# Performance work log

Measured on AMD Instinct MI355X. Metric: run time of the kernel, lower is better.

The kernel has to match this reference:

```python
import jax, jax.numpy as jnp
import numpy as np

N_HEADS = 8
D_EMBED = 512
D_HEAD = D_EMBED // N_HEADS


def setup_inputs() -> dict:
    key = jax.random.key(0)
    ks = jax.random.split(key, 5)
    s = 1.0 / np.sqrt(D_EMBED)
    return {
        "x": jax.random.normal(ks[0], (2, 4096, D_EMBED), dtype=jnp.float32),
        "in_proj_w": jax.random.normal(ks[1], (3 * D_EMBED, D_EMBED), dtype=jnp.float32) * s,
        "in_proj_b": jax.random.normal(ks[2], (3 * D_EMBED,), dtype=jnp.float32) * s,
        "out_proj_w": jax.random.normal(ks[3], (D_EMBED, D_EMBED), dtype=jnp.float32) * s,
        "out_proj_b": jax.random.normal(ks[4], (D_EMBED,), dtype=jnp.float32) * s,
    }


def reference(x, in_proj_w, in_proj_b, out_proj_w, out_proj_b):
    B, S, D = x.shape
    # in_proj: x @ W^T + b, then chunk into q, k, v
    qkv = jnp.einsum("bsd,ed->bse", x, in_proj_w) + in_proj_b  # [B,S,3D]
    q, k, v = jnp.split(qkv, 3, axis=-1)
    # [B,S,D] -> [B,H,S,dh]
    def heads(t):
        return t.reshape(B, S, N_HEADS, D_HEAD).transpose(0, 2, 1, 3)
    q, k, v = heads(q), heads(k), heads(v)
    scale = 1.0 / np.sqrt(D_HEAD).astype(np.float32)
    scores = jnp.einsum("bhqd,bhkd->bhqk", q, k) * scale  # [B,H,S,S]
    attn = jax.nn.softmax(scores, axis=-1)
    out = jnp.einsum("bhqk,bhkd->bhqd", attn, v)  # [B,H,S,dh]
    out = out.transpose(0, 2, 1, 3).reshape(B, S, D)
    return jnp.einsum("bsd,ed->bse", out, out_proj_w) + out_proj_b
```

## Files before the change

kernel.cpp:

```cpp
#include <hip/hip_runtime.h>
#include <cstdint>
#include <cstddef>

typedef __bf16 bf16x8 __attribute__((ext_vector_type(8)));
typedef float f32x4 __attribute__((ext_vector_type(4)));
typedef float f32x16 __attribute__((ext_vector_type(16)));
typedef unsigned int u32x4 __attribute__((ext_vector_type(4)));
typedef int i32x2 __attribute__((ext_vector_type(2)));
typedef unsigned short u16;
typedef unsigned short u16x8 __attribute__((ext_vector_type(8)));
typedef unsigned int u32;

#define S_LEN 4096
#define NH 8
#define DH 64
#define D_EMB 512
#define BATCH 2
#define M_ROWS 8192
#define GK 512
#define QSCALE 0.18033688011112042f

__device__ __forceinline__ u16 f2bf(float f) {
  u32 u = __builtin_bit_cast(u32, f);
  u += 0x7FFFu + ((u >> 16) & 1u);
  return (u16)(u >> 16);
}
__device__ __forceinline__ float bf2f(u16 v) {
  return __builtin_bit_cast(float, (u32)v << 16);
}
__device__ __forceinline__ u32 pk2(float a, float b) {
  union { __bf16 h[2]; u32 w; } u;
  u.h[0] = (__bf16)a;
  u.h[1] = (__bf16)b;
  return u.w;
}
__device__ __forceinline__ float fexp2(float x) {
#if __has_builtin(__builtin_amdgcn_exp2f)
  return __builtin_amdgcn_exp2f(x);
#else
  return __expf(x * 0.6931471805599453f);
#endif
}

__device__ __forceinline__ float xhalf_add(float v) {
#if __has_builtin(__builtin_amdgcn_permlane32_swap)
  const int a = (int)__builtin_bit_cast(u32, v);
  i32x2 r = __builtin_amdgcn_permlane32_swap(a, a, false, false);
  return __builtin_bit_cast(float, (u32)r.x) +
         __builtin_bit_cast(float, (u32)r.y);
#else
  return v + __shfl_xor(v, 32, 64);
#endif
}

#define MFMA32(a, b, c) __builtin_amdgcn_mfma_f32_32x32x16_bf16(a, b, c, 0, 0, 0)

#define GLD_LDS16(gsrc, ldst)                                                        \
  __builtin_amdgcn_global_load_lds(                                                  \
      (const __attribute__((address_space(1))) void*)(gsrc),                         \
      (__attribute__((address_space(3))) void*)(ldst), 16, 0, 0)

__global__ void detect_kernel(const u16* __restrict__ x, int* __restrict__ flag) {
  __shared__ int cnt;
  if (threadIdx.x == 0) cnt = 0;
  __syncthreads();
  int plaus = 0;
  for (int i = threadIdx.x; i < 2048; i += 256) {
    u16 u = x[2 * i];
    int ex = (u >> 7) & 0xFF;
    plaus += (ex >= 100 && ex <= 134) ? 1 : 0;
  }
  atomicAdd(&cnt, plaus);
  __syncthreads();
  if (threadIdx.x == 0) *flag = (cnt > 1024) ? 0 : 1;
}

__global__ void prep_kernel(const void* __restrict__ x, const void* __restrict__ wq,
                            const void* __restrict__ bq, const void* __restrict__ wo,
                            const void* __restrict__ bo,
                            u16* __restrict__ xb, u16* __restrict__ wqb,
                            u16* __restrict__ wob, float* __restrict__ bqf,
                            float* __restrict__ bof, const int* __restrict__ flag) {
  const bool f32 = (*flag != 0);
  const size_t i = (size_t)blockIdx.x * blockDim.x + threadIdx.x;
  if (i < (size_t)M_ROWS * D_EMB)
    xb[i] = f32 ? f2bf(((const float*)x)[i]) : ((const u16*)x)[i];
  if (i < (size_t)3 * D_EMB * D_EMB)
    wqb[i] = f32 ? f2bf(((const float*)wq)[i]) : ((const u16*)wq)[i];
  if (i < (size_t)D_EMB * D_EMB)
    wob[i] = f32 ? f2bf(((const float*)wo)[i]) : ((const u16*)wo)[i];
  if (i < 3 * D_EMB)
    bqf[i] = f32 ? ((const float*)bq)[i] : bf2f(((const u16*)bq)[i]);
  if (i < D_EMB)
    bof[i] = f32 ? ((const float*)bo)[i] : bf2f(((const u16*)bo)[i]);
}

template <int EPI>
__global__ __launch_bounds__(256, 3)
void gemm_bt(const u16* __restrict__ A, const u16* __restrict__ B, int N,
             const float* __restrict__ bias, u16* __restrict__ qout,
             u16* __restrict__ kout, u16* __restrict__ vout, u16* __restrict__ obf,
             float* __restrict__ of32, const int* __restrict__ flag) {
  __shared__ u16 As[128 * 64];
  __shared__ u16 Bs[128 * 64];
  const int tid = threadIdx.x;
  const int wave = tid >> 6, lane = tid & 63;
  const int m0 = blockIdx.x * 128;
  const int n0 = blockIdx.y * 128;
  const int wr = (wave >> 1) * 64, wc = (wave & 1) * 64;

  const int sr = wave * 8 + (lane >> 3);
  const int scb = (lane & 7) * 16;

  f32x4 acc[4][4] = {};

  for (int k0 = 0; k0 < GK; k0 += 64) {
#pragma unroll
    for (int i = 0; i < 4; ++i) {
      const int r = i * 32 + sr;
      const int sc = (scb ^ ((r & 7) << 4)) >> 1;
      GLD_LDS16(A + (size_t)(m0 + r) * GK + k0 + sc, As + i * 2048 + wave * 512);
    }
#pragma unroll
    for (int i = 0; i < 4; ++i) {
      const int r = i * 32 + sr;
      const int sc = (scb ^ ((r & 7) << 4)) >> 1;
      GLD_LDS16(B + (size_t)(n0 + r) * GK + k0 + sc, Bs + i * 2048 + wave * 512);
    }
    __syncthreads();
#pragma unroll
    for (int kk = 0; kk < 2; ++kk) {
      const int cb = kk * 64 + ((lane >> 4) << 4);
      bf16x8 a[4], b[4];
#pragma unroll
      for (int m = 0; m < 4; ++m) {
        const int r = wr + m * 16 + (lane & 15);
        a[m] = *(const bf16x8*)((const char*)As + r * 128 + (cb ^ ((r & 7) << 4)));
      }
#pragma unroll
      for (int n = 0; n < 4; ++n) {
        const int r = wc + n * 16 + (lane & 15);
        b[n] = *(const bf16x8*)((const char*)Bs + r * 128 + (cb ^ ((r & 7) << 4)));
      }
#pragma unroll
      for (int m = 0; m < 4; ++m)
#pragma unroll
        for (int n = 0; n < 4; ++n)
          acc[m][n] = __builtin_amdgcn_mfma_f32_16x16x32_bf16(a[m], b[n], acc[m][n], 0, 0, 0);
    }
    __syncthreads();
  }

  const bool f32out = (EPI == 1) && (*flag != 0);
#pragma unroll
  for (int n = 0; n < 4; ++n) {
    const int col = n0 + wc + n * 16 + (lane & 15);
    const float bv = bias[col];
#pragma unroll
    for (int m = 0; m < 4; ++m) {
#pragma unroll
      for (int r = 0; r < 4; ++r) {
        const int row = m0 + wr + m * 16 + ((lane >> 4) << 2) + r;
        float v = acc[m][n][r] + bv;
        if (EPI == 0) {
          const int bb = row >> 12, s = row & 4095;
          const int which = col >> 9, hc = col & 511;
          const int h = hc >> 6, d = hc & 63;
          const int bh = bb * NH + h;
          if (which == 2) {
            const int t16 = s >> 4, dblk = d >> 5;
            const int lane_ = ((s >> 3) & 1) * 32 + (d & 31);
            const int j = s & 7;
            vout[(((size_t)(bh * 256 + t16) * 2 + dblk) * 64 + lane_) * 8 + j] = f2bf(v);
          } else {
            const int t32 = s >> 5, dk = d >> 4;
            const int lane_ = ((d >> 3) & 1) * 32 + (s & 31);
            const int j = d & 7;
            u16* dst = (which == 0) ? qout : kout;
            const float vv = (which == 0) ? v * QSCALE : v;
            dst[(((size_t)(bh * 128 + t32) * 4 + dk) * 64 + lane_) * 8 + j] = f2bf(vv);
          }
        } else {
          if (f32out)
            of32[(size_t)row * D_EMB + col] = v;
          else
            obf[(size_t)row * D_EMB + col] = f2bf(v);
        }
      }
    }
  }
}

__global__ __launch_bounds__(256, 4)
void flash_attn(const u16* __restrict__ qfrag, const u16* __restrict__ kfrag,
                const u16* __restrict__ vfrag, u16* __restrict__ ao) {
  __shared__ float Ols[32][65];
  __shared__ float Lsh[4][32];

  const int phys = blockIdx.x;
  const int xcd = phys & 7, slot = phys >> 3;
  const int bh = xcd * 2 + (slot >> 7);
  const int qi = slot & 127;
  const int b = bh >> 3, h = bh & 7;
  const int q0 = qi * 32;

  const int lane = threadIdx.x & 63;
  const int hf = threadIdx.x >> 6;
  const int l31 = lane & 31, hi = lane >> 5;

  bf16x8 qf[4];
  {
    const u16* qb_ = qfrag + ((size_t)(bh * 128 + qi) * 4) * 512 + lane * 8;
#pragma unroll
    for (int dk = 0; dk < 4; ++dk) qf[dk] = *(const bf16x8*)(qb_ + dk * 512);
  }

  const u16* kptr = kfrag + (size_t)bh * (128 * 4 * 512) +
                    (size_t)(hf * 32) * 4 * 512 + lane * 8;
  const u16* vptr = vfrag + (size_t)bh * (256 * 2 * 512) +
                    (size_t)(hf * 64) * 2 * 512 + lane * 8;

  f32x16 accO0 = {}, accO1 = {};
  float lsum = 0.f;

#pragma unroll 1
  for (int it = 0; it < 32; ++it) {
    bf16x8 kf[4], vfA[2], vfB[2];
#pragma unroll
    for (int dk = 0; dk < 4; ++dk)
      kf[dk] = *(const bf16x8*)(kptr + dk * 512);
    vfA[0] = *(const bf16x8*)(vptr);
    vfB[0] = *(const bf16x8*)(vptr + 512);
    vfA[1] = *(const bf16x8*)(vptr + 1024);
    vfB[1] = *(const bf16x8*)(vptr + 1536);
    kptr += 2048;
    vptr += 2048;

    f32x16 s = {};
#pragma unroll
    for (int dk = 0; dk < 4; ++dk) s = MFMA32(kf[dk], qf[dk], s);

#pragma unroll
    for (int i = 0; i < 16; ++i) s[i] = fexp2(s[i]);

    float sm8[8];
#pragma unroll
    for (int i = 0; i < 8; ++i) sm8[i] = s[i] + s[i + 8];
    float sm4[4];
#pragma unroll
    for (int i = 0; i < 4; ++i) sm4[i] = sm8[i] + sm8[i + 4];
    const float sown = (sm4[0] + sm4[1]) + (sm4[2] + sm4[3]);
    lsum += xhalf_add(sown);

    u32 W0, W1, W2, W3;
#if __has_builtin(__builtin_amdgcn_permlane32_swap)
#define PACK8(P, B0)                                                            \
    {                                                                           \
      const u32 w0 = pk2(P[B0 + 0], P[B0 + 1]);                                 \
      const u32 w1 = pk2(P[B0 + 2], P[B0 + 3]);                                 \
      const u32 w2 = pk2(P[B0 + 4], P[B0 + 5]);                                 \
      const u32 w3 = pk2(P[B0 + 6], P[B0 + 7]);                                 \
      i32x2 rA = __builtin_amdgcn_permlane32_swap((int)w0, (int)w2, false, false); \
      i32x2 rB = __builtin_amdgcn_permlane32_swap((int)w1, (int)w3, false, false); \
      W0 = (u32)rA.x; W2 = (u32)rA.y;                                           \
      W1 = (u32)rB.x; W3 = (u32)rB.y;                                           \
    }
#else
#define PACK8(P, B0)                                                   \
    {                                                                  \
      const u32 w0 = pk2(P[B0 + 0], P[B0 + 1]);                        \
      const u32 w1 = pk2(P[B0 + 2], P[B0 + 3]);                        \
      const u32 w2 = pk2(P[B0 + 4], P[B0 + 5]);                        \
      const u32 w3 = pk2(P[B0 + 6], P[B0 + 7]);                        \
      const u32 rA = (u32)__shfl_xor((int)(hi ? w0 : w2), 32, 64);     \
      const u32 rB = (u32)__shfl_xor((int)(hi ? w1 : w3), 32, 64);     \
      W0 = hi ? rA : w0;                                               \
      W1 = hi ? rB : w1;                                               \
      W2 = hi ? w2 : rA;                                               \
      W3 = hi ? w3 : rB;                                               \
    }
#endif

    bf16x8 pa;
    PACK8(s, 0);
    pa = __builtin_bit_cast(bf16x8, (u32x4){W0, W1, W2, W3});
    accO0 = MFMA32(pa, vfA[0], accO0);
    accO1 = MFMA32(pa, vfB[0], accO1);
    PACK8(s, 8);
    pa = __builtin_bit_cast(bf16x8, (u32x4){W0, W1, W2, W3});
    accO0 = MFMA32(pa, vfA[1], accO0);
    accO1 = MFMA32(pa, vfB[1], accO1);
#undef PACK8
  }

  if (hi == 0) Lsh[hf][l31] = lsum;
  __syncthreads();
  const float L = (Lsh[0][l31] + Lsh[1][l31]) + (Lsh[2][l31] + Lsh[3][l31]);
  const float w = 1.0f / L;

#define DEPOSIT(OP)                                                    \
  {                                                                    \
    _Pragma("unroll")                                                  \
    for (int r = 0; r < 16; ++r) {                                     \
      const int qrow = (r & 3) + 8 * (r >> 2) + 4 * hi;                \
      Ols[qrow][l31] OP accO0[r];                                      \
      Ols[qrow][32 + l31] OP accO1[r];                                 \
    }                                                                  \
  }

  if (hf == 0) DEPOSIT(=);
  __syncthreads();
  if (hf == 1) DEPOSIT(+=);
  __syncthreads();
  if (hf == 2) DEPOSIT(+=);
  __syncthreads();
  if (hf == 3) {
#pragma unroll
    for (int r = 0; r < 16; ++r) {
      const int qrow = (r & 3) + 8 * (r >> 2) + 4 * hi;
      const float wr_ = __shfl(w, qrow, 64);
      const float o0 = (accO0[r] + Ols[qrow][l31]) * wr_;
      const float o1 = (accO1[r] + Ols[qrow][32 + l31]) * wr_;
      u16* orow = ao + (size_t)(b * S_LEN + q0 + qrow) * D_EMB + h * DH;
      orow[l31] = f2bf(o0);
      orow[32 + l31] = f2bf(o1);
    }
  }
#undef DEPOSIT
}

extern "C" void kernel_launch(void* const* d_in, const int* in_sizes, int n_in,
                              void* d_out, int out_size, void* d_ws, size_t ws_size,
                              hipStream_t stream) {
  char* w = (char*)d_ws;
  int* flag = (int*)w;
  u16* xb = (u16*)(w + 256);
  u16* wqb = (u16*)(w + 8388864);
  u16* wob = (u16*)(w + 9961728);
  float* bqf = (float*)(w + 10486016);
  float* bof = (float*)(w + 10492160);
  u16* qfr = (u16*)(w + 10494208);
  u16* kfr = (u16*)(w + 18882816);
  u16* vfr = (u16*)(w + 27271424);
  u16* ao = (u16*)(w + 35660032);

  detect_kernel<<<1, 256, 0, stream>>>((const u16*)d_in[0], flag);
  prep_kernel<<<16384, 256, 0, stream>>>(d_in[0], d_in[1], d_in[2], d_in[3], d_in[4],
                                         xb, wqb, wob, bqf, bof, flag);
  gemm_bt<0><<<dim3(64, 12), 256, 0, stream>>>(xb, wqb, 3 * D_EMB, bqf, qfr, kfr, vfr,
                                               nullptr, nullptr, flag);
  flash_attn<<<2048, 256, 0, stream>>>(qfr, kfr, vfr, ao);
  gemm_bt<1><<<dim3(64, 4), 256, 0, stream>>>(ao, wob, D_EMB, bof, nullptr, nullptr,
                                              nullptr, (u16*)d_out, (float*)d_out, flag);
}
```

Before: 147.0 us.

## Rebalance flash attention to 128-query blocks with 2-way KV split; skip bf16 copies

The attention kernel now launches 512 blocks of 512 threads. Each block has four query groups of 32 rows, and each group splits the keys across two waves that each walk 64 iterations. Before, every 32-query block split the keys four ways. The change cuts the cross-wave reduction to one shared-memory deposit and one barrier pair, and it lets the four query groups in a block share K/V loads through the cache. Separately, when the inputs are already bf16, the prep kernel no longer copies x and the weights, and the GEMMs read the raw inputs directly. The longer per-wave loop reduces parallelism per query, and the larger shared-memory footprint may limit occupancy.

```diff
diff --git a/kernel.cpp b/kernel.cpp
--- a/kernel.cpp
+++ b/kernel.cpp
@@ -83,26 +83,31 @@
                             float* __restrict__ bof, const int* __restrict__ flag) {
   const bool f32 = (*flag != 0);
   const size_t i = (size_t)blockIdx.x * blockDim.x + threadIdx.x;
-  if (i < (size_t)M_ROWS * D_EMB)
-    xb[i] = f32 ? f2bf(((const float*)x)[i]) : ((const u16*)x)[i];
-  if (i < (size_t)3 * D_EMB * D_EMB)
-    wqb[i] = f32 ? f2bf(((const float*)wq)[i]) : ((const u16*)wq)[i];
-  if (i < (size_t)D_EMB * D_EMB)
-    wob[i] = f32 ? f2bf(((const float*)wo)[i]) : ((const u16*)wo)[i];
-  if (i < 3 * D_EMB)
-    bqf[i] = f32 ? ((const float*)bq)[i] : bf2f(((const u16*)bq)[i]);
-  if (i < D_EMB)
-    bof[i] = f32 ? ((const float*)bo)[i] : bf2f(((const u16*)bo)[i]);
+  if (!f32) {
+    if (i < 3 * D_EMB) bqf[i] = bf2f(((const u16*)bq)[i]);
+    if (i < D_EMB) bof[i] = bf2f(((const u16*)bo)[i]);
+    return;
+  }
+  if (i < (size_t)M_ROWS * D_EMB) xb[i] = f2bf(((const float*)x)[i]);
+  if (i < (size_t)3 * D_EMB * D_EMB) wqb[i] = f2bf(((const float*)wq)[i]);
+  if (i < (size_t)D_EMB * D_EMB) wob[i] = f2bf(((const float*)wo)[i]);
+  if (i < 3 * D_EMB) bqf[i] = ((const float*)bq)[i];
+  if (i < D_EMB) bof[i] = ((const float*)bo)[i];
 }
 
 template <int EPI>
 __global__ __launch_bounds__(256, 3)
-void gemm_bt(const u16* __restrict__ A, const u16* __restrict__ B, int N,
+void gemm_bt(const u16* __restrict__ Acvt, const void* __restrict__ Araw,
+             const u16* __restrict__ Bcvt, const void* __restrict__ Braw, int N,
              const float* __restrict__ bias, u16* __restrict__ qout,
              u16* __restrict__ kout, u16* __restrict__ vout, u16* __restrict__ obf,
              float* __restrict__ of32, const int* __restrict__ flag) {
   __shared__ u16 As[128 * 64];
   __shared__ u16 Bs[128 * 64];
+  const bool f32in = (*flag != 0);
+  const u16* A = f32in ? Acvt : (const u16*)Araw;
+  const u16* B = f32in ? Bcvt : (const u16*)Braw;
+
   const int tid = threadIdx.x;
   const int wave = tid >> 6, lane = tid & 63;
   const int m0 = blockIdx.x * 128;
@@ -151,7 +156,7 @@
     __syncthreads();
   }
 
-  const bool f32out = (EPI == 1) && (*flag != 0);
+  const bool f32out = (EPI == 1) && f32in;
 #pragma unroll
   for (int n = 0; n < 4; ++n) {
     const int col = n0 + wc + n * 16 + (lane & 15);
@@ -191,40 +196,39 @@
   }
 }
 
-__global__ __launch_bounds__(256, 4)
+__global__ __launch_bounds__(512, 4)
 void flash_attn(const u16* __restrict__ qfrag, const u16* __restrict__ kfrag,
                 const u16* __restrict__ vfrag, u16* __restrict__ ao) {
-  __shared__ float Ols[32][65];
-  __shared__ float Lsh[4][32];
+  __shared__ float Ols[4][32][65];
+  __shared__ float Lsh[4][2][32];
 
   const int phys = blockIdx.x;
   const int xcd = phys & 7, slot = phys >> 3;
-  const int bh = xcd * 2 + (slot >> 7);
-  const int qi = slot & 127;
+  const int bh = xcd * 2 + (slot >> 5);
+  const int qt = slot & 31;
   const int b = bh >> 3, h = bh & 7;
-  const int q0 = qi * 32;
 
   const int lane = threadIdx.x & 63;
-  const int hf = threadIdx.x >> 6;
+  const int w8 = threadIdx.x >> 6;
+  const int g = w8 & 3, hf = w8 >> 2;
   const int l31 = lane & 31, hi = lane >> 5;
+  const int q0 = qt * 128 + g * 32;
 
   bf16x8 qf[4];
   {
-    const u16* qb_ = qfrag + ((size_t)(bh * 128 + qi) * 4) * 512 + lane * 8;
+    const u16* qb_ = qfrag + ((size_t)(bh * 128 + (q0 >> 5)) * 4) * 512 + lane * 8;
 #pragma unroll
     for (int dk = 0; dk < 4; ++dk) qf[dk] = *(const bf16x8*)(qb_ + dk * 512);
   }
 
-  const u16* kptr = kfrag + (size_t)bh * (128 * 4 * 512) +
-                    (size_t)(hf * 32) * 4 * 512 + lane * 8;
-  const u16* vptr = vfrag + (size_t)bh * (256 * 2 * 512) +
-                    (size_t)(hf * 64) * 2 * 512 + lane * 8;
+  const u16* kptr = kfrag + ((size_t)(bh * 128 + hf * 64) * 4) * 512 + lane * 8;
+  const u16* vptr = vfrag + ((size_t)(bh * 256 + hf * 128) * 2) * 512 + lane * 8;
 
   f32x16 accO0 = {}, accO1 = {};
   float lsum = 0.f;
 
 #pragma unroll 1
-  for (int it = 0; it < 32; ++it) {
+  for (int it = 0; it < 64; ++it) {
     bf16x8 kf[4], vfA[2], vfB[2];
 #pragma unroll
     for (int dk = 0; dk < 4; ++dk)
@@ -293,40 +297,32 @@
 #undef PACK8
   }
 
-  if (hi == 0) Lsh[hf][l31] = lsum;
+  if (hi == 0) Lsh[g][hf][l31] = lsum;
   __syncthreads();
-  const float L = (Lsh[0][l31] + Lsh[1][l31]) + (Lsh[2][l31] + Lsh[3][l31]);
+  const float L = Lsh[g][0][l31] + Lsh[g][1][l31];
   const float w = 1.0f / L;
 
-#define DEPOSIT(OP)                                                    \
-  {                                                                    \
-    _Pragma("unroll")                                                  \
-    for (int r = 0; r < 16; ++r) {                                     \
-      const int qrow = (r & 3) + 8 * (r >> 2) + 4 * hi;                \
-      Ols[qrow][l31] OP accO0[r];                                      \
-      Ols[qrow][32 + l31] OP accO1[r];                                 \
-    }                                                                  \
-  }
-
-  if (hf == 0) DEPOSIT(=);
+  if (hf == 0) {
+#pragma unroll
+    for (int r = 0; r < 16; ++r) {
+      const int qrow = (r & 3) + 8 * (r >> 2) + 4 * hi;
+      Ols[g][qrow][l31] = accO0[r];
+      Ols[g][qrow][32 + l31] = accO1[r];
+    }
+  }
   __syncthreads();
-  if (hf == 1) DEPOSIT(+=);
-  __syncthreads();
-  if (hf == 2) DEPOSIT(+=);
-  __syncthreads();
-  if (hf == 3) {
+  if (hf == 1) {
 #pragma unroll
     for (int r = 0; r < 16; ++r) {
       const int qrow = (r & 3) + 8 * (r >> 2) + 4 * hi;
       const float wr_ = __shfl(w, qrow, 64);
-      const float o0 = (accO0[r] + Ols[qrow][l31]) * wr_;
-      const float o1 = (accO1[r] + Ols[qrow][32 + l31]) * wr_;
+      const float o0 = (accO0[r] + Ols[g][qrow][l31]) * wr_;
+      const float o1 = (accO1[r] + Ols[g][qrow][32 + l31]) * wr_;
       u16* orow = ao + (size_t)(b * S_LEN + q0 + qrow) * D_EMB + h * DH;
       orow[l31] = f2bf(o0);
       orow[32 + l31] = f2bf(o1);
     }
   }
-#undef DEPOSIT
 }
 
 extern "C" void kernel_launch(void* const* d_in, const int* in_sizes, int n_in,
@@ -347,9 +343,11 @@
   detect_kernel<<<1, 256, 0, stream>>>((const u16*)d_in[0], flag);
   prep_kernel<<<16384, 256, 0, stream>>>(d_in[0], d_in[1], d_in[2], d_in[3], d_in[4],
                                          xb, wqb, wob, bqf, bof, flag);
-  gemm_bt<0><<<dim3(64, 12), 256, 0, stream>>>(xb, wqb, 3 * D_EMB, bqf, qfr, kfr, vfr,
-                                               nullptr, nullptr, flag);
-  flash_attn<<<2048, 256, 0, stream>>>(qfr, kfr, vfr, ao);
-  gemm_bt<1><<<dim3(64, 4), 256, 0, stream>>>(ao, wob, D_EMB, bof, nullptr, nullptr,
-                                              nullptr, (u16*)d_out, (float*)d_out, flag);
-}
+  gemm_bt<0><<<dim3(64, 12), 256, 0, stream>>>(xb, d_in[0], wqb, d_in[1], 3 * D_EMB,
+                                               bqf, qfr, kfr, vfr, nullptr, nullptr,
+                                               flag);
+  flash_attn<<<512, 512, 0, stream>>>(qfr, kfr, vfr, ao);
+  gemm_bt<1><<<dim3(64, 4), 256, 0, stream>>>(ao, ao, wob, d_in[3], D_EMB, bof,
+                                              nullptr, nullptr, nullptr,
+                                              (u16*)d_out, (float*)d_out, flag);
+}
```

Result: faster. 143.6 us (median of 2 runs) (-2.3%).
